# Optimization experiments

Measured on AMD Instinct MI355X. Metric: run time of the kernel, lower is better.

Reference implementation:

```python
import jax, jax.numpy as jnp
import numpy as np

N = 128        # n_neurons == neuron_dim (required by einsum 'bdn,ijn')
IN_FEAT = 4608  # grid_size**2 * embed_dim_doubled = 9 * 512
B = 32          # batch(4) * num_candidates(8)


def setup_inputs() -> dict:
    key = jax.random.key(0)
    ks = jax.random.split(key, 8)
    s_in = 1.0 / np.sqrt(IN_FEAT)
    s_d = 1.0 / np.sqrt(N)
    return {
        "x": jax.random.normal(ks[0], (B, IN_FEAT), jnp.float32),
        "input_proj_w": jax.random.uniform(ks[1], (N, IN_FEAT), jnp.float32, -s_in, s_in),
        "input_proj_b": jax.random.uniform(ks[2], (N,), jnp.float32, -s_in, s_in),
        "neuron_states": jax.random.normal(ks[3], (N, N), jnp.float32),
        "edge_vectors": jax.random.normal(ks[4], (N, N, N), jnp.float32),
        "recreate_w": jax.random.uniform(ks[5], (IN_FEAT, N), jnp.float32, -s_d, s_d),
        "recreate_b": jnp.zeros((IN_FEAT,), jnp.float32),
        "score_w": jax.random.uniform(ks[6], (1, N), jnp.float32, -s_d, s_d),
        "score_b": jnp.zeros((1,), jnp.float32),
        "grid_size": 3,
        "num_candidates": 8,
        "n_steps": 2,
    }


def reference(x, input_proj_w, input_proj_b, neuron_states, edge_vectors,
              recreate_w, recreate_b, score_w, score_b,
              grid_size, num_candidates, n_steps):
    bc = x.shape[0]                                   # batch * num_candidates
    embed_dim_doubled = x.shape[1] // (grid_size ** 2)
    n = neuron_states.shape[0]                        # == neuron_dim

    x_t = x @ input_proj_w.T + input_proj_b          # (B, d)
    # neuron_states: (n, d) -> states: (B, d, n), input added per feature channel
    states = neuron_states.T[None, :, :] + x_t[:, :, None]
    mask = 1.0 - jnp.eye(n, dtype=x.dtype)            # (n, n), no self term

    for _ in range(n_steps):
        # (B,d,n) x (n,n,n) -> (B,d,i,j): the O(B*d*n^2) intermediate
        T = jnp.einsum('bdn,ijn->bdij', states, edge_vectors)
        messages = jnp.einsum('bdij,bdn->bdi', T, states)  # (B, d, n)
        # literal broadcast of mask (1,n,n) against (B,d,n); valid since d==n
        messages = messages * mask[None, :, :]
        states = jax.nn.relu(messages)                     # (B, d, n)

    out = states[:, :, -1]                                 # (B, d)
    recreation = out @ recreate_w.T + recreate_b           # (B, IN_FEAT)
    scores = out @ score_w.T + score_b                     # (B, 1)

    bsz = bc // num_candidates
    recreation = recreation.reshape(bsz, num_candidates, grid_size ** 2, embed_dim_doubled)
    scores = scores.reshape(bsz, num_candidates)
    return recreation, scores
```

## Files before the change

kernel.cpp:

```cpp
#include <hip/hip_runtime.h>


#define KQ 1152

__device__ __forceinline__ float wave_reduce64(float v) {
#pragma unroll
  for (int m = 32; m >= 1; m >>= 1) v += __shfl_xor(v, m);
  return v;
}

#define WS_EJP 0
#define WS_E 65536
#define WS_CS 65664
#define WS_XT 65792
#define WS_AT 69888
#define WS_EJ127 86272
#define WS_OBD 86400

__global__ __launch_bounds__(256) void k1_pre(const float* __restrict__ ev,
                                              const float* __restrict__ ns,
                                              const float* __restrict__ x,
                                              const float* __restrict__ ipw,
                                              const float* __restrict__ ipb,
                                              float* __restrict__ ws) {
  __shared__ __align__(16) float4 sarr[256];
  int tid = threadIdx.x;
  int blk = blockIdx.x;
  if (blk < 512) {
    int i = blk >> 2, jc = blk & 3;
    int n4 = tid & 31, jg = tid >> 5;
    const float4* ev4 = (const float4*)ev;
    float4 acc = make_float4(0.f, 0.f, 0.f, 0.f);
#pragma unroll
    for (int jj = 0; jj < 4; ++jj) {
      int j = jc * 32 + jj * 8 + jg;
      float4 v = ev4[i * 4096 + j * 32 + n4];
      acc.x += v.x; acc.y += v.y; acc.z += v.z; acc.w += v.w;
    }
    sarr[tid] = acc;
    __syncthreads();
    if (tid < 32) {
      float4 s = sarr[tid];
#pragma unroll
      for (int k = 1; k < 8; ++k) {
        float4 v = sarr[tid + 32 * k];
        s.x += v.x; s.y += v.y; s.z += v.z; s.w += v.w;
      }
      ((float4*)(ws + WS_EJP))[(jc * 128 + i) * 32 + tid] = s;
    }
  } else if (blk < 1536) {
    int gw = (blk - 512) * 4 + (tid >> 6);
    int b = gw >> 7, d = gw & 127, lane = tid & 63;
    const float4* x4 = (const float4*)x;
    const float4* w4 = (const float4*)ipw;
    float acc = 0.f;
#pragma unroll 6
    for (int kq = lane; kq < KQ; kq += 64) {
      float4 xv = x4[b * KQ + kq];
      float4 wv = w4[d * KQ + kq];
      acc += xv.x * wv.x + xv.y * wv.y + xv.z * wv.z + xv.w * wv.w;
    }
    acc = wave_reduce64(acc);
    if (lane == 0) (ws + WS_XT)[b * 128 + d] = acc + ipb[d];
  } else {
    float* smem = (float*)sarr;
    int d = tid & 127, nh = tid >> 7;
    const float* Np = ns + nh * 64 * 128 + d;
    float acc = 0.f;
#pragma unroll 8
    for (int n = 0; n < 64; ++n) acc += Np[n * 128];
    smem[tid] = acc;
    __syncthreads();
    if (tid < 128) (ws + WS_CS)[tid] = smem[tid] + smem[tid + 128];
  }
}

__global__ __launch_bounds__(256) void k2_at(const float* __restrict__ ns,
                                             float* __restrict__ ws) {
  __shared__ float ej2[256];
  int tid = threadIdx.x;
  int i0 = blockIdx.x * 2;
  {
    int r = tid >> 7, n = tid & 127;
    const float* EJp = ws + WS_EJP;
    float v = EJp[(0 * 128 + i0 + r) * 128 + n] + EJp[(1 * 128 + i0 + r) * 128 + n] +
              EJp[(2 * 128 + i0 + r) * 128 + n] + EJp[(3 * 128 + i0 + r) * 128 + n];
    ej2[r * 128 + n] = v;
    if (i0 + r == 127) (ws + WS_EJ127)[n] = v;
  }
  __syncthreads();
  {
    int w = tid >> 6, l = tid & 63;
    if (w < 2) {
      float v = ej2[w * 128 + l] + ej2[w * 128 + 64 + l];
      v = wave_reduce64(v);
      if (l == 0) (ws + WS_E)[i0 + w] = v;
    }
  }
  int d = tid & 127, g = tid >> 7;
  float acc = 0.f;
#pragma unroll 8
  for (int n = 0; n < 128; ++n) acc += ej2[g * 128 + n] * ns[n * 128 + d];
  (ws + WS_AT)[d * 128 + i0 + g] = acc;
}

__global__ __launch_bounds__(512) void k3_steps(float* __restrict__ ws) {
  const float* xt = ws + WS_XT;
  const float* colsum = ws + WS_CS;
  const float* At = ws + WS_AT;
  const float* e = ws + WS_E;
  const float* ej127 = ws + WS_EJ127;
  float* obd = ws + WS_OBD;
  int gw = blockIdx.x * 8 + (threadIdx.x >> 6);
  int b = gw >> 7, d = gw & 127;
  int l = threadIdx.x & 63;
  float t = xt[b * 128 + d];
  float s0s = colsum[d] + 128.f * t;
  float sig = 0.f, y = 0.f;
#pragma unroll
  for (int m = 0; m < 2; ++m) {
    int i = l + (m << 6);
    float v = s0s * (At[d * 128 + i] + t * e[i]);
    v = (i == d) ? 0.f : v;
    v = fmaxf(v, 0.f);
    sig += v;
    y += ej127[i] * v;
  }
  sig = wave_reduce64(sig);
  y = wave_reduce64(y);
  if (l == 0) {
    float m2 = sig * y;
    if (d == 127) m2 = 0.f;
    obd[b * 128 + d] = fmaxf(m2, 0.f);
  }
}

__global__ __launch_bounds__(256) void k4_proj(const float* __restrict__ rw,
                                               const float* __restrict__ rb,
                                               const float* __restrict__ sw,
                                               const float* __restrict__ sb,
                                               const float* __restrict__ ws,
                                               float* __restrict__ out) {
  const float* obd = ws + WS_OBD;
  int tid = threadIdx.x;
  int blk = blockIdx.x;
  if (blk < 144) {
    __shared__ __align__(16) float rwlds[32 * 136];
    __shared__ float obdT[128 * 33];
    int f0 = blk * 32;
    const float4* rw4 = (const float4*)rw;
#pragma unroll
    for (int it = 0; it < 4; ++it) {
      int q = tid + 256 * it;
      int f = q >> 5, n4 = q & 31;
      *(float4*)&rwlds[f * 136 + n4 * 4] = rw4[f0 * 32 + q];
    }
#pragma unroll
    for (int it = 0; it < 16; ++it) {
      int q = tid + 256 * it;
      int b = q >> 7, d = q & 127;
      obdT[d * 33 + b] = obd[q];
    }
    __syncthreads();
    int f = tid >> 3, bg = tid & 7;
    float acc[4] = {0.f, 0.f, 0.f, 0.f};
#pragma unroll 4
    for (int d = 0; d < 128; ++d) {
      float w = rwlds[f * 136 + d];
#pragma unroll
      for (int k = 0; k < 4; ++k) acc[k] += w * obdT[d * 33 + bg * 4 + k];
    }
    float bias = rb[f0 + f];
#pragma unroll
    for (int k = 0; k < 4; ++k) out[(bg * 4 + k) * 4608 + f0 + f] = acc[k] + bias;
  } else {
    int b = tid >> 3, l8 = tid & 7;
    float acc = 0.f;
    for (int d = l8; d < 128; d += 8) acc += obd[b * 128 + d] * sw[d];
    acc += __shfl_xor(acc, 1);
    acc += __shfl_xor(acc, 2);
    acc += __shfl_xor(acc, 4);
    if (l8 == 0) out[147456 + b] = acc + sb[0];
  }
}

extern "C" void kernel_launch(void* const* d_in, const int* in_sizes, int n_in,
                              void* d_out, int out_size, void* d_ws, size_t ws_size,
                              hipStream_t stream) {
  const float* x   = (const float*)d_in[0];
  const float* ipw = (const float*)d_in[1];
  const float* ipb = (const float*)d_in[2];
  const float* ns  = (const float*)d_in[3];
  const float* ev  = (const float*)d_in[4];
  const float* rw  = (const float*)d_in[5];
  const float* rb  = (const float*)d_in[6];
  const float* sw  = (const float*)d_in[7];
  const float* sb  = (const float*)d_in[8];
  float* out = (float*)d_out;
  float* ws = (float*)d_ws;

  k1_pre<<<1537, 256, 0, stream>>>(ev, ns, x, ipw, ipb, ws);
  k2_at<<<64, 256, 0, stream>>>(ns, ws);
  k3_steps<<<512, 512, 0, stream>>>(ws);
  k4_proj<<<145, 256, 0, stream>>>(rw, rb, sw, sb, ws, out);
}
```

Measured before the change: 105.7 us.

## Fuse A-matrix precompute with step kernel and register-block input projection

Merges the edge-sum reduction, the A^T matvec, the column sum and the two-step recurrence into one kernel launched with one block per feature d. Each block rebuilds the full 128x128 edge-sum matrix in shared memory from the partials. The input projection now computes a 2x2 (batch x feature) tile per wave, so each x and W load is reused twice. This removes one launch and the workspace round-trips between the old k2 and k3, at the cost of every block redundantly reading and summing the 256KB of partials.

```diff
diff --git a/kernel.cpp b/kernel.cpp
--- a/kernel.cpp
+++ b/kernel.cpp
@@ -10,23 +10,17 @@
 }
 
 #define WS_EJP 0
-#define WS_E 65536
-#define WS_CS 65664
-#define WS_XT 65792
-#define WS_AT 69888
-#define WS_EJ127 86272
-#define WS_OBD 86400
+#define WS_XT 65536
+#define WS_OBD 69632
 
 __global__ __launch_bounds__(256) void k1_pre(const float* __restrict__ ev,
-                                              const float* __restrict__ ns,
                                               const float* __restrict__ x,
                                               const float* __restrict__ ipw,
                                               const float* __restrict__ ipb,
                                               float* __restrict__ ws) {
-  __shared__ __align__(16) float4 sarr[256];
-  int tid = threadIdx.x;
-  int blk = blockIdx.x;
+  int tid = threadIdx.x, blk = blockIdx.x;
   if (blk < 512) {
+    __shared__ __align__(16) float4 sarr[256];
     int i = blk >> 2, jc = blk & 3;
     int n4 = tid & 31, jg = tid >> 5;
     const float4* ev4 = (const float4*)ev;
@@ -48,94 +42,122 @@
       }
       ((float4*)(ws + WS_EJP))[(jc * 128 + i) * 32 + tid] = s;
     }
-  } else if (blk < 1536) {
+  } else {
     int gw = (blk - 512) * 4 + (tid >> 6);
-    int b = gw >> 7, d = gw & 127, lane = tid & 63;
+    int lane = tid & 63;
+    int b0 = (gw >> 6) << 1, d0 = (gw & 63) << 1;
     const float4* x4 = (const float4*)x;
     const float4* w4 = (const float4*)ipw;
-    float acc = 0.f;
+    float a00 = 0.f, a01 = 0.f, a10 = 0.f, a11 = 0.f;
 #pragma unroll 6
     for (int kq = lane; kq < KQ; kq += 64) {
-      float4 xv = x4[b * KQ + kq];
-      float4 wv = w4[d * KQ + kq];
-      acc += xv.x * wv.x + xv.y * wv.y + xv.z * wv.z + xv.w * wv.w;
-    }
-    acc = wave_reduce64(acc);
-    if (lane == 0) (ws + WS_XT)[b * 128 + d] = acc + ipb[d];
-  } else {
-    float* smem = (float*)sarr;
-    int d = tid & 127, nh = tid >> 7;
-    const float* Np = ns + nh * 64 * 128 + d;
-    float acc = 0.f;
-#pragma unroll 8
-    for (int n = 0; n < 64; ++n) acc += Np[n * 128];
-    smem[tid] = acc;
-    __syncthreads();
-    if (tid < 128) (ws + WS_CS)[tid] = smem[tid] + smem[tid + 128];
-  }
-}
-
-__global__ __launch_bounds__(256) void k2_at(const float* __restrict__ ns,
-                                             float* __restrict__ ws) {
-  __shared__ float ej2[256];
-  int tid = threadIdx.x;
-  int i0 = blockIdx.x * 2;
+      float4 xa = x4[b0 * KQ + kq];
+      float4 xb = x4[(b0 + 1) * KQ + kq];
+      float4 wa = w4[d0 * KQ + kq];
+      float4 wb = w4[(d0 + 1) * KQ + kq];
+      a00 += xa.x * wa.x + xa.y * wa.y + xa.z * wa.z + xa.w * wa.w;
+      a01 += xa.x * wb.x + xa.y * wb.y + xa.z * wb.z + xa.w * wb.w;
+      a10 += xb.x * wa.x + xb.y * wa.y + xb.z * wa.z + xb.w * wa.w;
+      a11 += xb.x * wb.x + xb.y * wb.y + xb.z * wb.z + xb.w * wb.w;
+    }
+    a00 = wave_reduce64(a00);
+    a01 = wave_reduce64(a01);
+    a10 = wave_reduce64(a10);
+    a11 = wave_reduce64(a11);
+    if (lane == 0) {
+      float* xt = ws + WS_XT;
+      xt[b0 * 128 + d0] = a00 + ipb[d0];
+      xt[b0 * 128 + d0 + 1] = a01 + ipb[d0 + 1];
+      xt[(b0 + 1) * 128 + d0] = a10 + ipb[d0];
+      xt[(b0 + 1) * 128 + d0 + 1] = a11 + ipb[d0 + 1];
+    }
+  }
+}
+
+#define EJS 129
+__global__ __launch_bounds__(256) void k2_fused(const float* __restrict__ ns,
+                                                float* __restrict__ ws) {
+  __shared__ float ej[128 * EJS];
+  __shared__ float nscol[128];
+  __shared__ float at2[2][128], e2[2][128];
+  __shared__ float At[128], Ev[128];
+  __shared__ float xts[32];
+  __shared__ float csum_s;
+  int tid = threadIdx.x, d = blockIdx.x;
+  if (tid < 128) nscol[tid] = ns[tid * 128 + d];
+  else if (tid < 160) xts[tid - 128] = (ws + WS_XT)[(tid - 128) * 128 + d];
   {
-    int r = tid >> 7, n = tid & 127;
-    const float* EJp = ws + WS_EJP;
-    float v = EJp[(0 * 128 + i0 + r) * 128 + n] + EJp[(1 * 128 + i0 + r) * 128 + n] +
-              EJp[(2 * 128 + i0 + r) * 128 + n] + EJp[(3 * 128 + i0 + r) * 128 + n];
-    ej2[r * 128 + n] = v;
-    if (i0 + r == 127) (ws + WS_EJ127)[n] = v;
+    int i = tid >> 1, h = tid & 1;
+    const float4* p0 = (const float4*)(ws + WS_EJP) + i * 32 + h * 16;
+#pragma unroll
+    for (int w = 0; w < 16; ++w) {
+      float4 v0 = p0[w];
+      float4 v1 = p0[4096 + w];
+      float4 v2 = p0[8192 + w];
+      float4 v3 = p0[12288 + w];
+      float* dst = &ej[i * EJS + h * 64 + w * 4];
+      dst[0] = v0.x + v1.x + v2.x + v3.x;
+      dst[1] = v0.y + v1.y + v2.y + v3.y;
+      dst[2] = v0.z + v1.z + v2.z + v3.z;
+      dst[3] = v0.w + v1.w + v2.w + v3.w;
+    }
   }
   __syncthreads();
   {
-    int w = tid >> 6, l = tid & 63;
-    if (w < 2) {
-      float v = ej2[w * 128 + l] + ej2[w * 128 + 64 + l];
-      v = wave_reduce64(v);
-      if (l == 0) (ws + WS_E)[i0 + w] = v;
-    }
-  }
-  int d = tid & 127, g = tid >> 7;
-  float acc = 0.f;
+    int i = tid & 127, h = tid >> 7;
+    float a = 0.f, es = 0.f;
+    const float* ejr = &ej[i * EJS + h * 64];
+    const float* nsr = &nscol[h * 64];
 #pragma unroll 8
-  for (int n = 0; n < 128; ++n) acc += ej2[g * 128 + n] * ns[n * 128 + d];
-  (ws + WS_AT)[d * 128 + i0 + g] = acc;
-}
-
-__global__ __launch_bounds__(512) void k3_steps(float* __restrict__ ws) {
-  const float* xt = ws + WS_XT;
-  const float* colsum = ws + WS_CS;
-  const float* At = ws + WS_AT;
-  const float* e = ws + WS_E;
-  const float* ej127 = ws + WS_EJ127;
+    for (int n = 0; n < 64; ++n) {
+      float v = ejr[n];
+      a += v * nsr[n];
+      es += v;
+    }
+    at2[h][i] = a;
+    e2[h][i] = es;
+  }
+  if (tid < 64) {
+    float cl = nscol[tid] + nscol[tid + 64];
+    cl = wave_reduce64(cl);
+    if (tid == 0) csum_s = cl;
+  }
+  __syncthreads();
+  if (tid < 128) {
+    At[tid] = at2[0][tid] + at2[1][tid];
+    Ev[tid] = e2[0][tid] + e2[1][tid];
+  }
+  __syncthreads();
+  float csum = csum_s;
+  int wv = tid >> 6, l = tid & 63;
+  const float* ej127 = &ej[127 * EJS];
   float* obd = ws + WS_OBD;
-  int gw = blockIdx.x * 8 + (threadIdx.x >> 6);
-  int b = gw >> 7, d = gw & 127;
-  int l = threadIdx.x & 63;
-  float t = xt[b * 128 + d];
-  float s0s = colsum[d] + 128.f * t;
-  float sig = 0.f, y = 0.f;
-#pragma unroll
-  for (int m = 0; m < 2; ++m) {
-    int i = l + (m << 6);
-    float v = s0s * (At[d * 128 + i] + t * e[i]);
-    v = (i == d) ? 0.f : v;
-    v = fmaxf(v, 0.f);
-    sig += v;
-    y += ej127[i] * v;
-  }
-  sig = wave_reduce64(sig);
-  y = wave_reduce64(y);
-  if (l == 0) {
-    float m2 = sig * y;
-    if (d == 127) m2 = 0.f;
-    obd[b * 128 + d] = fmaxf(m2, 0.f);
-  }
-}
-
-__global__ __launch_bounds__(256) void k4_proj(const float* __restrict__ rw,
+#pragma unroll
+  for (int bb = 0; bb < 8; ++bb) {
+    int b = wv * 8 + bb;
+    float t = xts[b];
+    float s0s = csum + 128.f * t;
+    float sig = 0.f, y = 0.f;
+#pragma unroll
+    for (int m = 0; m < 2; ++m) {
+      int i = l + (m << 6);
+      float v = s0s * (At[i] + t * Ev[i]);
+      v = (i == d) ? 0.f : v;
+      v = fmaxf(v, 0.f);
+      sig += v;
+      y += ej127[i] * v;
+    }
+    sig = wave_reduce64(sig);
+    y = wave_reduce64(y);
+    if (l == 0) {
+      float m2 = sig * y;
+      if (d == 127) m2 = 0.f;
+      obd[b * 128 + d] = fmaxf(m2, 0.f);
+    }
+  }
+}
+
+__global__ __launch_bounds__(256) void k3_proj(const float* __restrict__ rw,
                                                const float* __restrict__ rb,
                                                const float* __restrict__ sw,
                                                const float* __restrict__ sb,
@@ -199,8 +221,7 @@
   float* out = (float*)d_out;
   float* ws = (float*)d_ws;
 
-  k1_pre<<<1537, 256, 0, stream>>>(ev, ns, x, ipw, ipb, ws);
-  k2_at<<<64, 256, 0, stream>>>(ns, ws);
-  k3_steps<<<512, 512, 0, stream>>>(ws);
-  k4_proj<<<145, 256, 0, stream>>>(rw, rb, sw, sb, ws, out);
-}
+  k1_pre<<<768, 256, 0, stream>>>(ev, x, ipw, ipb, ws);
+  k2_fused<<<128, 256, 0, stream>>>(ns, ws);
+  k3_proj<<<145, 256, 0, stream>>>(rw, rb, sw, sb, ws, out);
+}
```

Measured after the change: 107.1 us. About the same (+1.3%).
